# Performance work log

Hardware: AMD Instinct MI355X
Metric: run time of the kernel (lower is better)

The kernel has to match this reference:

```python
import jax, jax.numpy as jnp
import numpy as np

B, S, D = 4, 2048, 768
H, E = 12, 64  # num_heads, head_size


def setup_inputs() -> dict:
    key = jax.random.key(0)
    ks = jax.random.split(key, 9)
    sd = 1.0 / np.sqrt(D)
    return {
        "x": jax.random.normal(ks[0], (B, S, D), dtype=jnp.float32),
        "Wq": jax.random.normal(ks[1], (H, D, E), dtype=jnp.float32) * sd,
        "bq": jax.random.normal(ks[2], (H, E), dtype=jnp.float32) * 0.02,
        "Wk": jax.random.normal(ks[3], (H, D, E), dtype=jnp.float32) * sd,
        "bk": jax.random.normal(ks[4], (H, E), dtype=jnp.float32) * 0.02,
        "Wv": jax.random.normal(ks[5], (H, D, E), dtype=jnp.float32) * sd,
        "bv": jax.random.normal(ks[6], (H, E), dtype=jnp.float32) * 0.02,
        "Wp": jax.random.normal(ks[7], (H * E, D), dtype=jnp.float32) * sd,
        "bp": jax.random.normal(ks[8], (D,), dtype=jnp.float32) * 0.02,
    }


def reference(x, Wq, bq, Wk, bk, Wv, bv, Wp, bp):
    # Batched multi-head QKV projections (replaces per-head Python loop)
    q = jnp.einsum("bsd,hde->bhse", x, Wq) + bq[None, :, None, :]
    k = jnp.einsum("bsd,hde->bhse", x, Wk) + bk[None, :, None, :]
    v = jnp.einsum("bsd,hde->bhse", x, Wv) + bv[None, :, None, :]
    scale = 1.0 / jnp.sqrt(jnp.asarray(E, dtype=x.dtype))
    # Full materialized attention matrix [B,H,S,S] as in the original module
    wei = jnp.einsum("bhqe,bhke->bhqk", q, k) * scale
    wei = jax.nn.softmax(wei, axis=-1)  # dropout=0 (eval) => identity
    out = jnp.einsum("bhqk,bhke->bhqe", wei, v)  # [B,H,S,E]
    # concat heads in head order then output projection
    out = out.transpose(0, 2, 1, 3).reshape(B, S, H * E)
    return out @ Wp + bp
```

## Files before the change

kernel.cpp:

```cpp
#include <hip/hip_runtime.h>
#include <cstddef>
#include <cstdint>

#define NB 4
#define NH 12
#define SQ 2048
#define DM 768
#define EH 64
#define MTOT (NB*SQ)
#define NQKV (NH*3*EH)

typedef __attribute__((ext_vector_type(8))) short short8;
typedef __attribute__((ext_vector_type(4))) float floatx4;

#define QSCALE 0.18033688011112042f

__device__ __forceinline__ unsigned short f2bf(float f) {
    unsigned int u = __float_as_uint(f);
    u += 0x7fffu + ((u >> 16) & 1u);
    return (unsigned short)(u >> 16);
}

#if __has_builtin(__builtin_amdgcn_exp2f)
__device__ __forceinline__ float fast_exp2(float x) { return __builtin_amdgcn_exp2f(x); }
#else
__device__ __forceinline__ float fast_exp2(float x) { return exp2f(x); }
#endif

#if __has_builtin(__builtin_amdgcn_cvt_pk_bf16_f32)
typedef __attribute__((ext_vector_type(2))) __bf16 bf16x2_t;
__device__ __forceinline__ unsigned int pack_bf16(float lo, float hi) {
    bf16x2_t v = __builtin_amdgcn_cvt_pk_bf16_f32(lo, hi);
    return __builtin_bit_cast(unsigned int, v);
}
#else
__device__ __forceinline__ unsigned int pack_bf16(float lo, float hi) {
    unsigned int u0 = __float_as_uint(lo) + 0x8000u;
    unsigned int u1 = __float_as_uint(hi) + 0x8000u;
    return __builtin_amdgcn_perm(u1, u0, 0x07060302u);
}
#endif
__device__ __forceinline__ short8 pack8(float a0,float a1,float a2,float a3,
                                        float b0,float b1,float b2,float b3) {
    union { unsigned int u[4]; short8 s; } cv;
    cv.u[0] = pack_bf16(a0, a1);
    cv.u[1] = pack_bf16(a2, a3);
    cv.u[2] = pack_bf16(b0, b1);
    cv.u[3] = pack_bf16(b2, b3);
    return cv.s;
}
__device__ __forceinline__ void gl_lds16(const void* g, void* l) {
    __builtin_amdgcn_global_load_lds(
        (const __attribute__((address_space(1))) unsigned int*)g,
        (__attribute__((address_space(3))) unsigned int*)l, 16, 0, 0);
}

#define CVT_A 1572864
#define CVT_B (CVT_A + 442368)
#define CVT_C (CVT_B + 147456)
#define CVT_D (CVT_C + 576)
__global__ __launch_bounds__(256) void convert_pack(
    const float* __restrict__ x,
    const float* __restrict__ Wq, const float* __restrict__ bq,
    const float* __restrict__ Wk, const float* __restrict__ bk,
    const float* __restrict__ Wv, const float* __restrict__ bv,
    const float* __restrict__ Wp,
    unsigned short* __restrict__ Xb, unsigned short* __restrict__ Wt,
    unsigned short* __restrict__ Wpt, float* __restrict__ bias_all)
{
    int t = blockIdx.x * 256 + threadIdx.x;
    if (t < CVT_A) {
        float4 v = ((const float4*)x)[t];
        ushort4 r; r.x = f2bf(v.x); r.y = f2bf(v.y); r.z = f2bf(v.z); r.w = f2bf(v.w);
        ((ushort4*)Xb)[t] = r;
    } else if (t < CVT_B) {
        int u = t - CVT_A;
        int n = u / 192, kc = (u % 192) * 4;
        int h = n / 192, rr = n % 192, wsel = rr >> 6, e = rr & 63;
        const float* W = (wsel == 0) ? Wq : ((wsel == 1) ? Wk : Wv);
        float sc = (wsel == 0) ? QSCALE : 1.0f;
        ushort4 r;
        r.x = f2bf(W[((size_t)h * DM + kc + 0) * EH + e] * sc);
        r.y = f2bf(W[((size_t)h * DM + kc + 1) * EH + e] * sc);
        r.z = f2bf(W[((size_t)h * DM + kc + 2) * EH + e] * sc);
        r.w = f2bf(W[((size_t)h * DM + kc + 3) * EH + e] * sc);
        ((ushort4*)Wt)[u] = r;
    } else if (t < CVT_C) {
        int u = t - CVT_B;
        int n = u / 192, kc = (u % 192) * 4;
        ushort4 r;
        r.x = f2bf(Wp[(size_t)(kc + 0) * DM + n]);
        r.y = f2bf(Wp[(size_t)(kc + 1) * DM + n]);
        r.z = f2bf(Wp[(size_t)(kc + 2) * DM + n]);
        r.w = f2bf(Wp[(size_t)(kc + 3) * DM + n]);
        ((ushort4*)Wpt)[u] = r;
    } else if (t < CVT_D) {
        int u = (t - CVT_C) * 4;
        #pragma unroll
        for (int j = 0; j < 4; j++) {
            int n = u + j;
            int h = n / 192, rr = n % 192, wsel = rr >> 6, e = rr & 63;
            const float* bs = (wsel == 0) ? bq : ((wsel == 1) ? bk : bv);
            bias_all[n] = bs[h * EH + e] * ((wsel == 0) ? QSCALE : 1.0f);
        }
    }
}

__global__ __launch_bounds__(256) void qkv_mfma(
    const unsigned short* __restrict__ Xb, const unsigned short* __restrict__ Wt,
    const float* __restrict__ bias_all,
    unsigned short* __restrict__ Qo, unsigned short* __restrict__ Kf,
    unsigned short* __restrict__ Vf)
{
    __shared__ unsigned short As[2][128 * 32];
    __shared__ unsigned short Bs[2][128 * 32];
    __shared__ unsigned short Ep[4][16 * 72];
    const int tid = threadIdx.x;
    const int w = tid >> 6, lane = tid & 63;
    const int l15 = lane & 15, quad = lane >> 4;
    const int wm = w & 1, wn = w >> 1;
    const int m0 = blockIdx.x * 128, n0 = blockIdx.y * 128;
    const int srow = w * 32 + (lane >> 2);
    const int pchunk = lane & 3;

    floatx4 acc[4][4];
    #pragma unroll
    for (int i = 0; i < 4; i++)
        #pragma unroll
        for (int j = 0; j < 4; j++) acc[i][j] = 0;

    #pragma unroll
    for (int c = 0; c < 2; c++) {
        int mr = srow + c * 16;
        int j = (pchunk - (mr >> 1)) & 3;
        gl_lds16(&Xb[(size_t)(m0 + mr) * DM + j * 8],
                 &As[0][w * 1024 + c * 512 + lane * 8]);
        gl_lds16(&Wt[(size_t)(n0 + mr) * DM + j * 8],
                 &Bs[0][w * 1024 + c * 512 + lane * 8]);
    }

    for (int kt = 0; kt < DM / 32; kt++) {
        const int cur = kt & 1;
        __syncthreads();
        if (kt + 1 < DM / 32) {
            int k0n = (kt + 1) * 32;
            #pragma unroll
            for (int c = 0; c < 2; c++) {
                int mr = srow + c * 16;
                int j = (pchunk - (mr >> 1)) & 3;
                gl_lds16(&Xb[(size_t)(m0 + mr) * DM + k0n + j * 8],
                         &As[cur ^ 1][w * 1024 + c * 512 + lane * 8]);
                gl_lds16(&Wt[(size_t)(n0 + mr) * DM + k0n + j * 8],
                         &Bs[cur ^ 1][w * 1024 + c * 512 + lane * 8]);
            }
        }
        short8 af[4], bf[4];
        #pragma unroll
        for (int mi = 0; mi < 4; mi++) {
            int row = wm * 64 + mi * 16 + l15;
            int pp = (quad + (row >> 1)) & 3;
            af[mi] = *(const short8*)&As[cur][row * 32 + pp * 8];
        }
        #pragma unroll
        for (int ni = 0; ni < 4; ni++) {
            int row = wn * 64 + ni * 16 + l15;
            int pp = (quad + (row >> 1)) & 3;
            bf[ni] = *(const short8*)&Bs[cur][row * 32 + pp * 8];
        }
        #pragma unroll
        for (int mi = 0; mi < 4; mi++)
            #pragma unroll
            for (int ni = 0; ni < 4; ni++)
                acc[mi][ni] = __builtin_amdgcn_mfma_f32_16x16x32_bf16(
                    af[mi], bf[ni], acc[mi][ni], 0, 0, 0);
    }
    __syncthreads();

    const int bB = m0 >> 11;
    const int ntb0 = n0 + wn * 64;
    const int h = ntb0 / 192, rr = ntb0 % 192;
    const int wsel = rr >> 6;
    const size_t bhbase = ((size_t)bB * NH + h) * (SQ * EH);
    const int sb_base = (m0 & 2047) + wm * 64;
    unsigned short* Ew = &Ep[w][0];
    float bvv[4];
    #pragma unroll
    for (int ni = 0; ni < 4; ni++) bvv[ni] = bias_all[ntb0 + ni * 16 + l15];

    if (wsel == 0) {
        #pragma unroll
        for (int mi = 0; mi < 4; mi++) {
            #pragma unroll
            for (int ni = 0; ni < 4; ni++)
                #pragma unroll
                for (int r = 0; r < 4; r++)
                    Ew[(quad * 4 + r) * 72 + ni * 16 + l15] =
                        f2bf(acc[mi][ni][r] + bvv[ni]);
            #pragma unroll
            for (int t = 0; t < 2; t++) {
                uint4 d = *(uint4*)&Ew[(t * 8 + (lane >> 3)) * 72 + (lane & 7) * 8];
                *(uint4*)&Qo[bhbase +
                    (size_t)(sb_base + mi * 16 + t * 8 + (lane >> 3)) * EH +
                    (lane & 7) * 8] = d;
            }
        }
    } else if (wsel == 1) {
        size_t tbase = bhbase + (size_t)(sb_base >> 6) * 4096;
        #pragma unroll
        for (int mi = 0; mi < 4; mi++) {
            #pragma unroll
            for (int ni = 0; ni < 4; ni++)
                #pragma unroll
                for (int r = 0; r < 4; r++)
                    Ew[(quad * 4 + r) * 72 + ni * 16 + l15] =
                        f2bf(acc[mi][ni][r] + bvv[ni]);
            #pragma unroll
            for (int t = 0; t < 2; t++) {
                uint4 d = *(uint4*)&Ew[l15 * 72 + t * 32 + quad * 8];
                *(uint4*)&Kf[tbase +
                    (size_t)((mi * 2 + t) * 64 + quad * 16 + l15) * 8] = d;
            }
        }
    } else {
        size_t tbase = bhbase + (size_t)(sb_base >> 6) * 4096;
        #pragma unroll
        for (int ni = 0; ni < 4; ni++) {
            #pragma unroll
            for (int mi = 0; mi < 4; mi++)
                #pragma unroll
                for (int r = 0; r < 4; r += 2) {
                    unsigned int pr = pack_bf16(acc[mi][ni][r]     + bvv[ni],
                                                acc[mi][ni][r + 1] + bvv[ni]);
                    *(unsigned int*)&Ew[l15 * 72 + quad * 16 + mi * 4 + r] = pr;
                }
            #pragma unroll
            for (int t = 0; t < 2; t++) {
                uint4 d = *(uint4*)&Ew[l15 * 72 + t * 32 + quad * 8];
                int unit = (ni * 2 + (quad & 1)) * 64 + ((quad >> 1) + 2 * t) * 16 + l15;
                *(uint4*)&Vf[tbase + (size_t)unit * 8] = d;
            }
        }
    }
}

__global__ __launch_bounds__(256, 3) void attn_mfma(
    const unsigned short* __restrict__ Q, const unsigned short* __restrict__ Kf,
    const unsigned short* __restrict__ Vf, unsigned short* __restrict__ O)
{
    __shared__ unsigned short Ks[2][4096];
    __shared__ unsigned short Vs[2][4096];
    const int tid = threadIdx.x;
    const int w = tid >> 6, lane = tid & 63;
    const int l15 = lane & 15, quad = lane >> 4;
    const int bh = blockIdx.x;
    const int b = bh / NH, h = bh % NH;
    const int q0 = blockIdx.y * 128;

    const unsigned short* Qb = Q + (size_t)bh * SQ * EH;
    const unsigned short* Kb = Kf + (size_t)bh * SQ * EH;
    const unsigned short* Vb = Vf + (size_t)bh * SQ * EH;

    short8 qf[2][2];
    #pragma unroll
    for (int qh = 0; qh < 2; qh++)
        #pragma unroll
        for (int kh = 0; kh < 2; kh++)
            qf[qh][kh] = *(const short8*)
                &Qb[(size_t)(q0 + w * 32 + qh * 16 + l15) * EH + kh * 32 + quad * 8];

    short8 ones;
    #pragma unroll
    for (int j = 0; j < 8; j++) ones[j] = (short)0x3F80;
    const floatx4 fzero = 0;

    floatx4 o[2][4], l_acc[2];
    #pragma unroll
    for (int qh = 0; qh < 2; qh++) {
        l_acc[qh] = 0;
        #pragma unroll
        for (int nb = 0; nb < 4; nb++) o[qh][nb] = 0;
    }

    const int seg = w * 2;
    #pragma unroll
    for (int c = 0; c < 2; c++) {
        gl_lds16(&Kb[(seg + c) * 512 + lane * 8], &Ks[0][(seg + c) * 512 + lane * 8]);
        gl_lds16(&Vb[(seg + c) * 512 + lane * 8], &Vs[0][(seg + c) * 512 + lane * 8]);
    }

    #pragma unroll 2
    for (int kb = 0; kb < SQ / 64; kb++) {
        const int cur = kb & 1;
        __syncthreads();
        if (kb + 1 < SQ / 64) {
            const unsigned short* Kn = Kb + (size_t)(kb + 1) * 4096;
            const unsigned short* Vn = Vb + (size_t)(kb + 1) * 4096;
            #pragma unroll
            for (int c = 0; c < 2; c++) {
                gl_lds16(&Kn[(seg + c) * 512 + lane * 8],
                         &Ks[cur ^ 1][(seg + c) * 512 + lane * 8]);
                gl_lds16(&Vn[(seg + c) * 512 + lane * 8],
                         &Vs[cur ^ 1][(seg + c) * 512 + lane * 8]);
            }
        }
        short8 kf[4][2];
        #pragma unroll
        for (int nb = 0; nb < 4; nb++)
            #pragma unroll
            for (int kh = 0; kh < 2; kh++)
                kf[nb][kh] = *(const short8*)&Ks[cur][((nb * 2 + kh) * 64 + lane) * 8];
        floatx4 s[2][4];
        #pragma unroll
        for (int qh = 0; qh < 2; qh++)
            #pragma unroll
            for (int nb = 0; nb < 4; nb++) {
                floatx4 z = __builtin_amdgcn_mfma_f32_16x16x32_bf16(
                    kf[nb][0], qf[qh][0], fzero, 0, 0, 0);
                s[qh][nb] = __builtin_amdgcn_mfma_f32_16x16x32_bf16(
                    kf[nb][1], qf[qh][1], z, 0, 0, 0);
            }
        short8 pa[2][2];
        #pragma unroll
        for (int qh = 0; qh < 2; qh++) {
            float p[4][4];
            #pragma unroll
            for (int nb = 0; nb < 4; nb++)
                #pragma unroll
                for (int r = 0; r < 4; r++)
                    p[nb][r] = fast_exp2(s[qh][nb][r]);
            pa[qh][0] = pack8(p[0][0], p[0][1], p[0][2], p[0][3],
                              p[1][0], p[1][1], p[1][2], p[1][3]);
            pa[qh][1] = pack8(p[2][0], p[2][1], p[2][2], p[2][3],
                              p[3][0], p[3][1], p[3][2], p[3][3]);
            l_acc[qh] = __builtin_amdgcn_mfma_f32_16x16x32_bf16(pa[qh][0], ones, l_acc[qh], 0, 0, 0);
            l_acc[qh] = __builtin_amdgcn_mfma_f32_16x16x32_bf16(pa[qh][1], ones, l_acc[qh], 0, 0, 0);
        }
        short8 vf[4][2];
        #pragma unroll
        for (int eb = 0; eb < 4; eb++)
            #pragma unroll
            for (int kh = 0; kh < 2; kh++)
                vf[eb][kh] = *(const short8*)&Vs[cur][((eb * 2 + kh) * 64 + lane) * 8];
        #pragma unroll
        for (int qh = 0; qh < 2; qh++)
            #pragma unroll
            for (int eb = 0; eb < 4; eb++) {
                o[qh][eb] = __builtin_amdgcn_mfma_f32_16x16x32_bf16(pa[qh][0], vf[eb][0], o[qh][eb], 0, 0, 0);
                o[qh][eb] = __builtin_amdgcn_mfma_f32_16x16x32_bf16(pa[qh][1], vf[eb][1], o[qh][eb], 0, 0, 0);
            }
    }

    #pragma unroll
    for (int qh = 0; qh < 2; qh++)
        #pragma unroll
        for (int r = 0; r < 4; r++) {
            float inv = 1.0f / l_acc[qh][r];
            int sidx = q0 + w * 32 + qh * 16 + quad * 4 + r;
            size_t base = (((size_t)b * SQ + sidx) * NH + h) * EH + l15;
            O[base +  0] = f2bf(o[qh][0][r] * inv);
            O[base + 16] = f2bf(o[qh][1][r] * inv);
            O[base + 32] = f2bf(o[qh][2][r] * inv);
            O[base + 48] = f2bf(o[qh][3][r] * inv);
        }
}

__global__ __launch_bounds__(256) void proj_mfma(
    const unsigned short* __restrict__ Ab, const unsigned short* __restrict__ Wpt,
    const float* __restrict__ bp, float* __restrict__ C)
{
    __shared__ unsigned short As[2][64 * 32];
    __shared__ unsigned short Bs[2][128 * 32];
    __shared__ float Epf[4][16 * 68];
    const int tid = threadIdx.x;
    const int w = tid >> 6, lane = tid & 63;
    const int l15 = lane & 15, quad = lane >> 4;
    const int wm = w & 1, wn = w >> 1;
    const int m0 = blockIdx.x * 64, n0 = blockIdx.y * 128;
    const int pchunk = lane & 3;

    floatx4 acc[2][4];
    #pragma unroll
    for (int i = 0; i < 2; i++)
        #pragma unroll
        for (int j = 0; j < 4; j++) acc[i][j] = 0;

    {
        int mr = w * 16 + (lane >> 2);
        int j = (pchunk - (mr >> 1)) & 3;
        gl_lds16(&Ab[(size_t)(m0 + mr) * DM + j * 8], &As[0][w * 512 + lane * 8]);
    }
    #pragma unroll
    for (int c = 0; c < 2; c++) {
        int nr = w * 32 + c * 16 + (lane >> 2);
        int j = (pchunk - (nr >> 1)) & 3;
        gl_lds16(&Wpt[(size_t)(n0 + nr) * DM + j * 8],
                 &Bs[0][w * 1024 + c * 512 + lane * 8]);
    }

    for (int kt = 0; kt < DM / 32; kt++) {
        const int cur = kt & 1;
        __syncthreads();
        if (kt + 1 < DM / 32) {
            int k0n = (kt + 1) * 32;
            {
                int mr = w * 16 + (lane >> 2);
                int j = (pchunk - (mr >> 1)) & 3;
                gl_lds16(&Ab[(size_t)(m0 + mr) * DM + k0n + j * 8],
                         &As[cur ^ 1][w * 512 + lane * 8]);
            }
            #pragma unroll
            for (int c = 0; c < 2; c++) {
                int nr = w * 32 + c * 16 + (lane >> 2);
                int j = (pchunk - (nr >> 1)) & 3;
                gl_lds16(&Wpt[(size_t)(n0 + nr) * DM + k0n + j * 8],
                         &Bs[cur ^ 1][w * 1024 + c * 512 + lane * 8]);
            }
        }
        short8 af[2], bf[4];
        #pragma unroll
        for (int mi = 0; mi < 2; mi++) {
            int row = wm * 32 + mi * 16 + l15;
            int pp = (quad + (row >> 1)) & 3;
            af[mi] = *(const short8*)&As[cur][row * 32 + pp * 8];
        }
        #pragma unroll
        for (int ni = 0; ni < 4; ni++) {
            int row = wn * 64 + ni * 16 + l15;
            int pp = (quad + (row >> 1)) & 3;
            bf[ni] = *(const short8*)&Bs[cur][row * 32 + pp * 8];
        }
        #pragma unroll
        for (int mi = 0; mi < 2; mi++)
            #pragma unroll
            for (int ni = 0; ni < 4; ni++)
                acc[mi][ni] = __builtin_amdgcn_mfma_f32_16x16x32_bf16(
                    af[mi], bf[ni], acc[mi][ni], 0, 0, 0);
    }
    __syncthreads();

    float* Ewf = &Epf[w][0];
    float bvv[4];
    #pragma unroll
    for (int ni = 0; ni < 4; ni++) bvv[ni] = bp[n0 + wn * 64 + ni * 16 + l15];
    #pragma unroll
    for (int mi = 0; mi < 2; mi++) {
        #pragma unroll
        for (int ni = 0; ni < 4; ni++)
            #pragma unroll
            for (int r = 0; r < 4; r++)
                Ewf[(quad * 4 + r) * 68 + ni * 16 + l15] = acc[mi][ni][r] + bvv[ni];
        #pragma unroll
        for (int t = 0; t < 4; t++) {
            float4 d = *(float4*)&Ewf[(t * 4 + quad) * 68 + l15 * 4];
            *(float4*)&C[(size_t)(m0 + wm * 32 + mi * 16 + t * 4 + quad) * DM +
                         n0 + wn * 64 + l15 * 4] = d;
        }
    }
}

extern "C" void kernel_launch(void* const* d_in, const int* in_sizes, int n_in,
                              void* d_out, int out_size, void* d_ws, size_t ws_size,
                              hipStream_t stream) {
    const float* x  = (const float*)d_in[0];
    const float* Wq = (const float*)d_in[1];
    const float* bq = (const float*)d_in[2];
    const float* Wk = (const float*)d_in[3];
    const float* bk = (const float*)d_in[4];
    const float* Wv = (const float*)d_in[5];
    const float* bv = (const float*)d_in[6];
    const float* Wp = (const float*)d_in[7];
    const float* bp = (const float*)d_in[8];
    float* out = (float*)d_out;

    const size_t QKV_ELEMS = (size_t)NB * NH * SQ * EH;
    unsigned short* Qb   = (unsigned short*)d_ws;
    unsigned short* Kfb  = Qb + QKV_ELEMS;
    unsigned short* Vfb  = Kfb + QKV_ELEMS;
    unsigned short* Abuf = Vfb + QKV_ELEMS;
    unsigned short* Xb   = Abuf + QKV_ELEMS;
    unsigned short* Wtb  = Xb + QKV_ELEMS;
    unsigned short* Wptb = Wtb + (size_t)NQKV * DM;
    float* bias_all      = (float*)(Wptb + (size_t)DM * DM);

    convert_pack<<<(CVT_D + 255) / 256, 256, 0, stream>>>(
        x, Wq, bq, Wk, bk, Wv, bv, Wp, Xb, Wtb, Wptb, bias_all);
    qkv_mfma<<<dim3(MTOT / 128, NQKV / 128), 256, 0, stream>>>(
        Xb, Wtb, bias_all, Qb, Kfb, Vfb);
    attn_mfma<<<dim3(NB * NH, SQ / 128), 256, 0, stream>>>(Qb, Kfb, Vfb, Abuf);
    proj_mfma<<<dim3(MTOT / 64, DM / 128), 256, 0, stream>>>(Abuf, Wptb, bp, out);
}
```

Before: 229.4 us.

## Triple-buffer K/V tiles in attention with manual waitcnt barriers and MFMA priority

The attention kernel moves from double to triple buffering of the K/V tiles in LDS. Loads are issued two tiles ahead, and the end-of-iteration sync becomes an explicit s_waitcnt vmcnt(4) plus s_barrier, so the newest prefetch can stay in flight. V fragment reads are hoisted next to the K reads, and the MFMA sections are wrapped in s_setprio to favour matrix issue across waves. LDS use rises to 48KB per block, which may limit occupancy under launch_bounds(256,3), and the hand-written waitcnt counts rely on the exact number of outstanding loads.

```diff
diff --git a/kernel.cpp b/kernel.cpp
--- a/kernel.cpp
+++ b/kernel.cpp
@@ -247,8 +247,8 @@
     const unsigned short* __restrict__ Q, const unsigned short* __restrict__ Kf,
     const unsigned short* __restrict__ Vf, unsigned short* __restrict__ O)
 {
-    __shared__ unsigned short Ks[2][4096];
-    __shared__ unsigned short Vs[2][4096];
+    __shared__ unsigned short Ks[3 * 4096];
+    __shared__ unsigned short Vs[3 * 4096];
     const int tid = threadIdx.x;
     const int w = tid >> 6, lane = tid & 63;
     const int l15 = lane & 15, quad = lane >> 4;
@@ -284,32 +284,49 @@
     const int seg = w * 2;
     #pragma unroll
     for (int c = 0; c < 2; c++) {
-        gl_lds16(&Kb[(seg + c) * 512 + lane * 8], &Ks[0][(seg + c) * 512 + lane * 8]);
-        gl_lds16(&Vb[(seg + c) * 512 + lane * 8], &Vs[0][(seg + c) * 512 + lane * 8]);
-    }
-
-    #pragma unroll 2
+        gl_lds16(&Kb[(seg + c) * 512 + lane * 8], &Ks[(seg + c) * 512 + lane * 8]);
+        gl_lds16(&Vb[(seg + c) * 512 + lane * 8], &Vs[(seg + c) * 512 + lane * 8]);
+    }
+    asm volatile("" ::: "memory");
+    #pragma unroll
+    for (int c = 0; c < 2; c++) {
+        gl_lds16(&Kb[4096 + (seg + c) * 512 + lane * 8],
+                 &Ks[4096 + (seg + c) * 512 + lane * 8]);
+        gl_lds16(&Vb[4096 + (seg + c) * 512 + lane * 8],
+                 &Vs[4096 + (seg + c) * 512 + lane * 8]);
+    }
+    asm volatile("s_waitcnt vmcnt(4)\n\ts_barrier" ::: "memory");
+
+    int cur_off = 0;
     for (int kb = 0; kb < SQ / 64; kb++) {
-        const int cur = kb & 1;
-        __syncthreads();
-        if (kb + 1 < SQ / 64) {
-            const unsigned short* Kn = Kb + (size_t)(kb + 1) * 4096;
-            const unsigned short* Vn = Vb + (size_t)(kb + 1) * 4096;
+        if (kb + 2 < SQ / 64) {
+            int nxt_off = cur_off + 8192;
+            if (nxt_off >= 12288) nxt_off -= 12288;
+            const unsigned short* Kn = Kb + (size_t)(kb + 2) * 4096;
+            const unsigned short* Vn = Vb + (size_t)(kb + 2) * 4096;
             #pragma unroll
             for (int c = 0; c < 2; c++) {
                 gl_lds16(&Kn[(seg + c) * 512 + lane * 8],
-                         &Ks[cur ^ 1][(seg + c) * 512 + lane * 8]);
+                         &Ks[nxt_off + (seg + c) * 512 + lane * 8]);
                 gl_lds16(&Vn[(seg + c) * 512 + lane * 8],
-                         &Vs[cur ^ 1][(seg + c) * 512 + lane * 8]);
-            }
-        }
-        short8 kf[4][2];
+                         &Vs[nxt_off + (seg + c) * 512 + lane * 8]);
+            }
+        }
+
+        short8 kf[4][2], vf[4][2];
         #pragma unroll
         for (int nb = 0; nb < 4; nb++)
             #pragma unroll
             for (int kh = 0; kh < 2; kh++)
-                kf[nb][kh] = *(const short8*)&Ks[cur][((nb * 2 + kh) * 64 + lane) * 8];
+                kf[nb][kh] = *(const short8*)&Ks[cur_off + ((nb * 2 + kh) * 64 + lane) * 8];
+        #pragma unroll
+        for (int eb = 0; eb < 4; eb++)
+            #pragma unroll
+            for (int kh = 0; kh < 2; kh++)
+                vf[eb][kh] = *(const short8*)&Vs[cur_off + ((eb * 2 + kh) * 64 + lane) * 8];
+
         floatx4 s[2][4];
+        __builtin_amdgcn_s_setprio(1);
         #pragma unroll
         for (int qh = 0; qh < 2; qh++)
             #pragma unroll
@@ -319,6 +336,8 @@
                 s[qh][nb] = __builtin_amdgcn_mfma_f32_16x16x32_bf16(
                     kf[nb][1], qf[qh][1], z, 0, 0, 0);
             }
+        __builtin_amdgcn_s_setprio(0);
+
         short8 pa[2][2];
         #pragma unroll
         for (int qh = 0; qh < 2; qh++) {
@@ -332,15 +351,14 @@
                               p[1][0], p[1][1], p[1][2], p[1][3]);
             pa[qh][1] = pack8(p[2][0], p[2][1], p[2][2], p[2][3],
                               p[3][0], p[3][1], p[3][2], p[3][3]);
+        }
+
+        __builtin_amdgcn_s_setprio(1);
+        #pragma unroll
+        for (int qh = 0; qh < 2; qh++) {
             l_acc[qh] = __builtin_amdgcn_mfma_f32_16x16x32_bf16(pa[qh][0], ones, l_acc[qh], 0, 0, 0);
             l_acc[qh] = __builtin_amdgcn_mfma_f32_16x16x32_bf16(pa[qh][1], ones, l_acc[qh], 0, 0, 0);
         }
-        short8 vf[4][2];
-        #pragma unroll
-        for (int eb = 0; eb < 4; eb++)
-            #pragma unroll
-            for (int kh = 0; kh < 2; kh++)
-                vf[eb][kh] = *(const short8*)&Vs[cur][((eb * 2 + kh) * 64 + lane) * 8];
         #pragma unroll
         for (int qh = 0; qh < 2; qh++)
             #pragma unroll
@@ -348,6 +366,15 @@
                 o[qh][eb] = __builtin_amdgcn_mfma_f32_16x16x32_bf16(pa[qh][0], vf[eb][0], o[qh][eb], 0, 0, 0);
                 o[qh][eb] = __builtin_amdgcn_mfma_f32_16x16x32_bf16(pa[qh][1], vf[eb][1], o[qh][eb], 0, 0, 0);
             }
+        __builtin_amdgcn_s_setprio(0);
+
+        if (kb + 2 < SQ / 64) {
+            asm volatile("s_waitcnt vmcnt(4)\n\ts_barrier" ::: "memory");
+        } else if (kb + 1 < SQ / 64) {
+            asm volatile("s_waitcnt vmcnt(0)\n\ts_barrier" ::: "memory");
+        }
+        cur_off += 4096;
+        if (cur_off >= 12288) cur_off = 0;
     }
 
     #pragma unroll
```

Result: no change. 230.4 us (+0.4%).

## Split attention KV range across wave pairs with 64-row Q tiles and LDS reduction

Applied to the files above, without the earlier changes.

The attention kernel now assigns each wave 64 query rows, up from 32, and splits the key/value sequence between two wave groups that process alternating 64-key tiles. This is backed by a 4-stage K/V LDS ring and a final LDS reduction of the partial O and row-sum accumulators. Each K/V fragment read from LDS is reused across more MFMAs, and s_setprio hints are added around the MFMA blocks. In exchange, register pressure is higher (occupancy bound lowered from 3 to 2 blocks per CU), LDS use is doubled, and there is an extra reduction epilogue with barriers.

```diff
diff --git a/kernel.cpp b/kernel.cpp
--- a/kernel.cpp
+++ b/kernel.cpp
@@ -243,15 +243,17 @@
     }
 }
 
-__global__ __launch_bounds__(256, 3) void attn_mfma(
+__global__ __launch_bounds__(256, 2) void attn_mfma(
     const unsigned short* __restrict__ Q, const unsigned short* __restrict__ Kf,
     const unsigned short* __restrict__ Vf, unsigned short* __restrict__ O)
 {
-    __shared__ unsigned short Ks[2][4096];
-    __shared__ unsigned short Vs[2][4096];
+    __shared__ unsigned short Ks[4][4096];
+    __shared__ unsigned short Vs[4][4096];
     const int tid = threadIdx.x;
     const int w = tid >> 6, lane = tid & 63;
     const int l15 = lane & 15, quad = lane >> 4;
+    const int wq = w & 1;
+    const int wk = w >> 1;
     const int bh = blockIdx.x;
     const int b = bh / NH, h = bh % NH;
     const int q0 = blockIdx.y * 128;
@@ -260,108 +262,137 @@
     const unsigned short* Kb = Kf + (size_t)bh * SQ * EH;
     const unsigned short* Vb = Vf + (size_t)bh * SQ * EH;
 
-    short8 qf[2][2];
-    #pragma unroll
-    for (int qh = 0; qh < 2; qh++)
+    short8 qf[4][2];
+    #pragma unroll
+    for (int qh = 0; qh < 4; qh++)
         #pragma unroll
         for (int kh = 0; kh < 2; kh++)
             qf[qh][kh] = *(const short8*)
-                &Qb[(size_t)(q0 + w * 32 + qh * 16 + l15) * EH + kh * 32 + quad * 8];
+                &Qb[(size_t)(q0 + wq * 64 + qh * 16 + l15) * EH + kh * 32 + quad * 8];
 
     short8 ones;
     #pragma unroll
     for (int j = 0; j < 8; j++) ones[j] = (short)0x3F80;
     const floatx4 fzero = 0;
 
-    floatx4 o[2][4], l_acc[2];
-    #pragma unroll
-    for (int qh = 0; qh < 2; qh++) {
+    floatx4 o[4][4], l_acc[4];
+    #pragma unroll
+    for (int qh = 0; qh < 4; qh++) {
         l_acc[qh] = 0;
         #pragma unroll
         for (int nb = 0; nb < 4; nb++) o[qh][nb] = 0;
     }
 
-    const int seg = w * 2;
-    #pragma unroll
-    for (int c = 0; c < 2; c++) {
-        gl_lds16(&Kb[(seg + c) * 512 + lane * 8], &Ks[0][(seg + c) * 512 + lane * 8]);
-        gl_lds16(&Vb[(seg + c) * 512 + lane * 8], &Vs[0][(seg + c) * 512 + lane * 8]);
-    }
-
-    #pragma unroll 2
-    for (int kb = 0; kb < SQ / 64; kb++) {
-        const int cur = kb & 1;
-        __syncthreads();
-        if (kb + 1 < SQ / 64) {
-            const unsigned short* Kn = Kb + (size_t)(kb + 1) * 4096;
-            const unsigned short* Vn = Vb + (size_t)(kb + 1) * 4096;
-            #pragma unroll
-            for (int c = 0; c < 2; c++) {
-                gl_lds16(&Kn[(seg + c) * 512 + lane * 8],
-                         &Ks[cur ^ 1][(seg + c) * 512 + lane * 8]);
-                gl_lds16(&Vn[(seg + c) * 512 + lane * 8],
-                         &Vs[cur ^ 1][(seg + c) * 512 + lane * 8]);
-            }
-        }
-        short8 kf[4][2];
+    #pragma unroll
+    for (int c = 0; c < 4; c++) {
+        int sg = wq * 4 + c;
+        gl_lds16(&Kb[(size_t)wk * 4096 + sg * 512 + lane * 8],
+                 &Ks[wk][sg * 512 + lane * 8]);
+        gl_lds16(&Vb[(size_t)wk * 4096 + sg * 512 + lane * 8],
+                 &Vs[wk][sg * 512 + lane * 8]);
+    }
+    asm volatile("s_waitcnt vmcnt(0)\n\ts_barrier" ::: "memory");
+
+    for (int j = 0; j < SQ / 128; j++) {
+        const int tj = 2 * j + wk;
+        const int bc = tj & 3;
+        if (j + 1 < SQ / 128) {
+            const int tn = tj + 2, bn = bc ^ 2;
+            #pragma unroll
+            for (int c = 0; c < 4; c++) {
+                int sg = wq * 4 + c;
+                gl_lds16(&Kb[(size_t)tn * 4096 + sg * 512 + lane * 8],
+                         &Ks[bn][sg * 512 + lane * 8]);
+                gl_lds16(&Vb[(size_t)tn * 4096 + sg * 512 + lane * 8],
+                         &Vs[bn][sg * 512 + lane * 8]);
+            }
+        }
+        short8 kf[4][2], vf[4][2];
         #pragma unroll
         for (int nb = 0; nb < 4; nb++)
             #pragma unroll
             for (int kh = 0; kh < 2; kh++)
-                kf[nb][kh] = *(const short8*)&Ks[cur][((nb * 2 + kh) * 64 + lane) * 8];
-        floatx4 s[2][4];
-        #pragma unroll
-        for (int qh = 0; qh < 2; qh++)
+                kf[nb][kh] = *(const short8*)&Ks[bc][((nb * 2 + kh) * 64 + lane) * 8];
+        #pragma unroll
+        for (int eb = 0; eb < 4; eb++)
+            #pragma unroll
+            for (int kh = 0; kh < 2; kh++)
+                vf[eb][kh] = *(const short8*)&Vs[bc][((eb * 2 + kh) * 64 + lane) * 8];
+
+        #pragma unroll
+        for (int qh = 0; qh < 4; qh++) {
+            floatx4 s[4];
+            __builtin_amdgcn_s_setprio(1);
             #pragma unroll
             for (int nb = 0; nb < 4; nb++) {
                 floatx4 z = __builtin_amdgcn_mfma_f32_16x16x32_bf16(
                     kf[nb][0], qf[qh][0], fzero, 0, 0, 0);
-                s[qh][nb] = __builtin_amdgcn_mfma_f32_16x16x32_bf16(
+                s[nb] = __builtin_amdgcn_mfma_f32_16x16x32_bf16(
                     kf[nb][1], qf[qh][1], z, 0, 0, 0);
             }
-        short8 pa[2][2];
-        #pragma unroll
-        for (int qh = 0; qh < 2; qh++) {
+            __builtin_amdgcn_s_setprio(0);
             float p[4][4];
             #pragma unroll
             for (int nb = 0; nb < 4; nb++)
                 #pragma unroll
                 for (int r = 0; r < 4; r++)
-                    p[nb][r] = fast_exp2(s[qh][nb][r]);
-            pa[qh][0] = pack8(p[0][0], p[0][1], p[0][2], p[0][3],
-                              p[1][0], p[1][1], p[1][2], p[1][3]);
-            pa[qh][1] = pack8(p[2][0], p[2][1], p[2][2], p[2][3],
-                              p[3][0], p[3][1], p[3][2], p[3][3]);
-            l_acc[qh] = __builtin_amdgcn_mfma_f32_16x16x32_bf16(pa[qh][0], ones, l_acc[qh], 0, 0, 0);
-            l_acc[qh] = __builtin_amdgcn_mfma_f32_16x16x32_bf16(pa[qh][1], ones, l_acc[qh], 0, 0, 0);
-        }
-        short8 vf[4][2];
-        #pragma unroll
-        for (int eb = 0; eb < 4; eb++)
-            #pragma unroll
-            for (int kh = 0; kh < 2; kh++)
-                vf[eb][kh] = *(const short8*)&Vs[cur][((eb * 2 + kh) * 64 + lane) * 8];
-        #pragma unroll
-        for (int qh = 0; qh < 2; qh++)
+                    p[nb][r] = fast_exp2(s[nb][r]);
+            short8 pa0 = pack8(p[0][0], p[0][1], p[0][2], p[0][3],
+                               p[1][0], p[1][1], p[1][2], p[1][3]);
+            short8 pa1 = pack8(p[2][0], p[2][1], p[2][2], p[2][3],
+                               p[3][0], p[3][1], p[3][2], p[3][3]);
+            __builtin_amdgcn_s_setprio(1);
+            l_acc[qh] = __builtin_amdgcn_mfma_f32_16x16x32_bf16(pa0, ones, l_acc[qh], 0, 0, 0);
+            l_acc[qh] = __builtin_amdgcn_mfma_f32_16x16x32_bf16(pa1, ones, l_acc[qh], 0, 0, 0);
             #pragma unroll
             for (int eb = 0; eb < 4; eb++) {
-                o[qh][eb] = __builtin_amdgcn_mfma_f32_16x16x32_bf16(pa[qh][0], vf[eb][0], o[qh][eb], 0, 0, 0);
-                o[qh][eb] = __builtin_amdgcn_mfma_f32_16x16x32_bf16(pa[qh][1], vf[eb][1], o[qh][eb], 0, 0, 0);
-            }
-    }
-
-    #pragma unroll
-    for (int qh = 0; qh < 2; qh++)
-        #pragma unroll
-        for (int r = 0; r < 4; r++) {
-            float inv = 1.0f / l_acc[qh][r];
-            int sidx = q0 + w * 32 + qh * 16 + quad * 4 + r;
-            size_t base = (((size_t)b * SQ + sidx) * NH + h) * EH + l15;
-            O[base +  0] = f2bf(o[qh][0][r] * inv);
-            O[base + 16] = f2bf(o[qh][1][r] * inv);
-            O[base + 32] = f2bf(o[qh][2][r] * inv);
-            O[base + 48] = f2bf(o[qh][3][r] * inv);
-        }
+                o[qh][eb] = __builtin_amdgcn_mfma_f32_16x16x32_bf16(pa0, vf[eb][0], o[qh][eb], 0, 0, 0);
+                o[qh][eb] = __builtin_amdgcn_mfma_f32_16x16x32_bf16(pa1, vf[eb][1], o[qh][eb], 0, 0, 0);
+            }
+            __builtin_amdgcn_s_setprio(0);
+        }
+        if (j + 1 < SQ / 128)
+            asm volatile("s_waitcnt vmcnt(0)\n\ts_barrier" ::: "memory");
+    }
+
+    __syncthreads();
+    float* Xo = (float*)&Ks[0][0];
+    float* Xl = (float*)&Vs[0][0];
+    if (wk == 1) {
+        float* po = Xo + wq * 4096;
+        float* pl = Xl + wq * 1024;
+        #pragma unroll
+        for (int qh = 0; qh < 4; qh++) {
+            #pragma unroll
+            for (int eb = 0; eb < 4; eb++)
+                *(floatx4*)&po[((qh * 4 + eb) * 64 + lane) * 4] = o[qh][eb];
+            *(floatx4*)&pl[(qh * 64 + lane) * 4] = l_acc[qh];
+        }
+    }
+    __syncthreads();
+    if (wk == 0) {
+        float* po = Xo + wq * 4096;
+        float* pl = Xl + wq * 1024;
+        #pragma unroll
+        for (int qh = 0; qh < 4; qh++) {
+            #pragma unroll
+            for (int eb = 0; eb < 4; eb++)
+                o[qh][eb] += *(floatx4*)&po[((qh * 4 + eb) * 64 + lane) * 4];
+            l_acc[qh] += *(floatx4*)&pl[(qh * 64 + lane) * 4];
+        }
+        #pragma unroll
+        for (int qh = 0; qh < 4; qh++)
+            #pragma unroll
+            for (int r = 0; r < 4; r++) {
+                float inv = 1.0f / l_acc[qh][r];
+                int sidx = q0 + wq * 64 + qh * 16 + quad * 4 + r;
+                size_t base = (((size_t)b * SQ + sidx) * NH + h) * EH + l15;
+                O[base +  0] = f2bf(o[qh][0][r] * inv);
+                O[base + 16] = f2bf(o[qh][1][r] * inv);
+                O[base + 32] = f2bf(o[qh][2][r] * inv);
+                O[base + 48] = f2bf(o[qh][3][r] * inv);
+            }
+    }
 }
 
 __global__ __launch_bounds__(256) void proj_mfma(
```

Result: slower. 236.9 us (+3.3%).
